# Performance work log

Measured on AMD Instinct MI355X. Metric: run time of the kernel, lower is better.

## Reference

```python
import jax
import jax.numpy as jnp
import numpy as np

N = 1024   # n_neurons (input size == hidden size)
L = 2      # n_layers of the stacked nn.RNN
T = 8      # n_tsteps (number of chained RNN+Linear blocks)
B = 1024   # x.shape[0]; acts as the RNN sequence length (batch=1 inside nn.RNN)


def setup_inputs() -> dict:
    key = jax.random.key(0)
    ks = jax.random.split(key, 7)
    s = 1.0 / np.sqrt(N)  # torch default init bound for RNN/Linear with fan_in=N
    x = jax.random.normal(ks[0], (B, T, N), dtype=jnp.float32)
    rnn_Wih = jax.random.uniform(ks[1], (T, L, N, N), minval=-s, maxval=s, dtype=jnp.float32)
    rnn_Whh = jax.random.uniform(ks[2], (T, L, N, N), minval=-s, maxval=s, dtype=jnp.float32)
    rnn_bih = jax.random.uniform(ks[3], (T, L, N), minval=-s, maxval=s, dtype=jnp.float32)
    rnn_bhh = jax.random.uniform(ks[4], (T, L, N), minval=-s, maxval=s, dtype=jnp.float32)
    lin_W = jax.random.uniform(ks[5], (T, N, N), minval=-s, maxval=s, dtype=jnp.float32)
    lin_b = jax.random.uniform(ks[6], (T, N), minval=-s, maxval=s, dtype=jnp.float32)
    return {"x": x, "rnn_Wih": rnn_Wih, "rnn_Whh": rnn_Whh,
            "rnn_bih": rnn_bih, "rnn_bhh": rnn_bhh,
            "lin_W": lin_W, "lin_b": lin_b}


def _rnn_layer(seq, Wih, Whh, bih, bhh):
    """Single tanh-RNN layer over sequence `seq` [S, N] with batch=1, h0=0."""
    def step(h, xt):
        h_new = jnp.tanh(xt @ Wih.T + bih + h @ Whh.T + bhh)
        return h_new, h_new
    _, out = jax.lax.scan(step, jnp.zeros((Wih.shape[0],), seq.dtype), seq)
    return out  # [S, N]


def reference(x, rnn_Wih, rnn_Whh, rnn_bih, rnn_bhh, lin_W, lin_b):
    # x: [B, T, N]. Torch code feeds x[:, 0, :] (shape [B, 1, N]) into nn.RNN
    # (batch_first=False), so B is the sequence length and batch size is 1.
    n_tsteps, n_layers = rnn_Wih.shape[0], rnn_Wih.shape[1]
    seq = x[:, 0, :]  # [B, N]
    outs = []
    for t in range(n_tsteps):
        for l in range(n_layers):
            seq = _rnn_layer(seq, rnn_Wih[t, l], rnn_Whh[t, l],
                             rnn_bih[t, l], rnn_bhh[t, l])
        seq = seq @ lin_W[t].T + lin_b[t]  # nn.Linear
        outs.append(seq)
    return jnp.stack(outs, axis=1)  # [B, T, N]
```

## Files before the change

### kernel.cpp

```cpp
#include <hip/hip_runtime.h>
#include <hip/hip_fp16.h>

#define NN 1024
#define NST 16

typedef _Float16 v2h __attribute__((ext_vector_type(2)));
typedef _Float16 f16x8 __attribute__((ext_vector_type(8)));
typedef float f32x4 __attribute__((ext_vector_type(4)));
typedef unsigned int uint;
typedef unsigned long long u64;
typedef unsigned int u32x4 __attribute__((ext_vector_type(4)));

__device__ __half g_W[NST][NN][2048];
__device__ float g_bias[NST][NN];
__device__ u64 g_S[NST][NN][512];
__device__ float g_Hout[8][NN * NN];
__device__ _Float16 g_Wih16F[7][NN * NN];
__device__ _Float16 g_linW16[8][NN * NN];

__device__ __forceinline__ v2h as_v2h(uint u) {
  union { uint u; v2h h; } c; c.u = u; return c.h;
}
__device__ __forceinline__ uint pk2(float a, float b) {
  union { v2h h; uint u; } c; c.h.x = (_Float16)a; c.h.y = (_Float16)b; return c.u;
}
__device__ __forceinline__ int swzu(int u) {
  return (u & ~7) | ((u + (u >> 3)) & 7);
}
__device__ __forceinline__ u32x4 ld_opaque16(const __half* p) {
  u32x4 r;
  asm volatile("global_load_dwordx4 %0, %1, off" : "=v"(r) : "v"(p));
  return r;
}
__device__ __forceinline__ float fdot4(u32x4 w, u32x4 v, float a) {
  a = __builtin_amdgcn_fdot2(as_v2h(w.x), as_v2h(v.x), a, false);
  a = __builtin_amdgcn_fdot2(as_v2h(w.y), as_v2h(v.y), a, false);
  a = __builtin_amdgcn_fdot2(as_v2h(w.z), as_v2h(v.z), a, false);
  a = __builtin_amdgcn_fdot2(as_v2h(w.w), as_v2h(v.w), a, false);
  return a;
}
__device__ __forceinline__ float dpp_reduce16(float v) {
  int t;
  t = __builtin_amdgcn_update_dpp(0, __float_as_int(v), 0x111, 0xF, 0xF, true); v += __int_as_float(t);
  t = __builtin_amdgcn_update_dpp(0, __float_as_int(v), 0x112, 0xF, 0xF, true); v += __int_as_float(t);
  t = __builtin_amdgcn_update_dpp(0, __float_as_int(v), 0x114, 0xF, 0xF, true); v += __int_as_float(t);
  t = __builtin_amdgcn_update_dpp(0, __float_as_int(v), 0x118, 0xF, 0xF, true); v += __int_as_float(t);
  return v;
}

__global__ void k_init() {
  const size_t n = (size_t)NST * NN * 512;
  size_t i = (size_t)blockIdx.x * blockDim.x + threadIdx.x;
  const size_t stride = (size_t)gridDim.x * blockDim.x;
  u64* p = &g_S[0][0][0];
  for (; i < n; i += stride) p[i] = 0ull;
}

__global__ void k_pack(const float* __restrict__ Wih, const float* __restrict__ Whh,
                       const float* __restrict__ linW) {
  const size_t total = (size_t)NST * NN * NN;
  const size_t stride = (size_t)gridDim.x * blockDim.x;
  for (size_t i = (size_t)blockIdx.x * blockDim.x + threadIdx.x; i < total; i += stride) {
    const int st = (int)(i >> 20);
    const int m = (int)(i >> 10) & 1023;
    const int k = (int)i & 1023;
    g_W[st][m][1024 + k] = __float2half(Whh[i]);
    const int t = st >> 1, l = st & 1;
    if (l == 1 || t == 0) g_W[st][m][k] = __float2half(Wih[i]);
    else g_Wih16F[t - 1][(size_t)m * NN + k] = (_Float16)Wih[i];
  }
  const size_t ltotal = (size_t)8 * NN * NN;
  _Float16* lw = &g_linW16[0][0];
  for (size_t i = (size_t)blockIdx.x * blockDim.x + threadIdx.x; i < ltotal; i += stride)
    lw[i] = (_Float16)linW[i];
}

#define GPAD 40

__global__ __launch_bounds__(256) void k_fold(int dummy) {
  const int tm1 = blockIdx.z;
  const int st = (tm1 + 1) * 2;
  const _Float16* A = &g_Wih16F[tm1][0];
  const _Float16* B = &g_linW16[tm1][0];
  __shared__ _Float16 sA[128 * GPAD];
  __shared__ _Float16 sB[128 * GPAD];
  const int tid = threadIdx.x;
  const int bm = blockIdx.y << 7, bn = blockIdx.x << 7;
  const int lane = tid & 63, wid = tid >> 6;
  const int wm = wid >> 1, wn = wid & 1;
  const int lr = lane & 15, kc = (lane >> 4) << 3;
  f32x4 acc[4][4] = {};
  const int arow = tid >> 1, ahalf = tid & 1;
  const int bj = tid >> 3, bcs = tid & 7;

  for (int k0 = 0; k0 < NN; k0 += 32) {
    __syncthreads();
    {
      const u32x4 a0 = *(const u32x4*)&A[(size_t)(bm + arow) * NN + k0 + 16 * ahalf];
      const u32x4 a1 = *(const u32x4*)&A[(size_t)(bm + arow) * NN + k0 + 16 * ahalf + 8];
      u32x4* dst = (u32x4*)&sA[arow * GPAD + 16 * ahalf];
      dst[0] = a0; dst[1] = a1;
      union { u32x4 v; _Float16 h[8]; } ua, ub;
      ua.v = *(const u32x4*)&B[(size_t)(k0 + bj) * NN + bn + 16 * bcs];
      ub.v = *(const u32x4*)&B[(size_t)(k0 + bj) * NN + bn + 16 * bcs + 8];
      #pragma unroll
      for (int q = 0; q < 8; ++q) sB[(16 * bcs + q) * GPAD + bj] = ua.h[q];
      #pragma unroll
      for (int q = 0; q < 8; ++q) sB[(16 * bcs + 8 + q) * GPAD + bj] = ub.h[q];
    }
    __syncthreads();
    f16x8 af[4], bf[4];
    #pragma unroll
    for (int f = 0; f < 4; ++f) {
      af[f] = *(const f16x8*)&sA[(wm * 64 + f * 16 + lr) * GPAD + kc];
      bf[f] = *(const f16x8*)&sB[(wn * 64 + f * 16 + lr) * GPAD + kc];
    }
    #pragma unroll
    for (int fm = 0; fm < 4; ++fm)
      #pragma unroll
      for (int fn = 0; fn < 4; ++fn)
        acc[fm][fn] = __builtin_amdgcn_mfma_f32_16x16x32_f16(af[fm], bf[fn], acc[fm][fn], 0, 0, 0);
  }
  const int orow = (lane >> 4) << 2, ocol = lane & 15;
  #pragma unroll
  for (int fm = 0; fm < 4; ++fm)
    #pragma unroll
    for (int fn = 0; fn < 4; ++fn) {
      const int gr = bm + wm * 64 + fm * 16 + orow;
      const int gc = bn + wn * 64 + fn * 16 + ocol;
      #pragma unroll
      for (int r = 0; r < 4; ++r)
        g_W[st][gr + r][gc] = __float2half(acc[fm][fn][r]);
    }
}

__global__ __launch_bounds__(256) void k_out(const float* __restrict__ linb,
                                             float* __restrict__ out) {
  const int t = blockIdx.z;
  const float* A = &g_Hout[t][0];
  const _Float16* B = &g_linW16[t][0];
  __shared__ _Float16 sA[128 * GPAD];
  __shared__ _Float16 sB[128 * GPAD];
  const int tid = threadIdx.x;
  const int bm = blockIdx.y << 7, bn = blockIdx.x << 7;
  const int lane = tid & 63, wid = tid >> 6;
  const int wm = wid >> 1, wn = wid & 1;
  const int lr = lane & 15, kc = (lane >> 4) << 3;
  f32x4 acc[4][4] = {};
  const int arow = tid >> 1, ahalf = tid & 1;

  for (int k0 = 0; k0 < NN; k0 += 32) {
    __syncthreads();
    {
      const float* srcA = &A[(size_t)(bm + arow) * NN + k0 + 16 * ahalf];
      const float4 f0 = *(const float4*)&srcA[0];
      const float4 f1 = *(const float4*)&srcA[4];
      const float4 f2 = *(const float4*)&srcA[8];
      const float4 f3 = *(const float4*)&srcA[12];
      u32x4 o0, o1;
      o0.x = pk2(f0.x, f0.y); o0.y = pk2(f0.z, f0.w);
      o0.z = pk2(f1.x, f1.y); o0.w = pk2(f1.z, f1.w);
      o1.x = pk2(f2.x, f2.y); o1.y = pk2(f2.z, f2.w);
      o1.z = pk2(f3.x, f3.y); o1.w = pk2(f3.z, f3.w);
      u32x4* dstA = (u32x4*)&sA[arow * GPAD + 16 * ahalf];
      dstA[0] = o0; dstA[1] = o1;
      const u32x4 b0 = *(const u32x4*)&B[(size_t)(bn + arow) * NN + k0 + 16 * ahalf];
      const u32x4 b1 = *(const u32x4*)&B[(size_t)(bn + arow) * NN + k0 + 16 * ahalf + 8];
      u32x4* dstB = (u32x4*)&sB[arow * GPAD + 16 * ahalf];
      dstB[0] = b0; dstB[1] = b1;
    }
    __syncthreads();
    f16x8 af[4], bf[4];
    #pragma unroll
    for (int f = 0; f < 4; ++f) {
      af[f] = *(const f16x8*)&sA[(wm * 64 + f * 16 + lr) * GPAD + kc];
      bf[f] = *(const f16x8*)&sB[(wn * 64 + f * 16 + lr) * GPAD + kc];
    }
    #pragma unroll
    for (int fm = 0; fm < 4; ++fm)
      #pragma unroll
      for (int fn = 0; fn < 4; ++fn)
        acc[fm][fn] = __builtin_amdgcn_mfma_f32_16x16x32_f16(af[fm], bf[fn], acc[fm][fn], 0, 0, 0);
  }
  const int orow = (lane >> 4) << 2, ocol = lane & 15;
  #pragma unroll
  for (int fm = 0; fm < 4; ++fm)
    #pragma unroll
    for (int fn = 0; fn < 4; ++fn) {
      const int gr = bm + wm * 64 + fm * 16 + orow;
      const int gc = bn + wn * 64 + fn * 16 + ocol;
      const float lb = linb[(size_t)t * NN + gc];
      #pragma unroll
      for (int r = 0; r < 4; ++r)
        out[(size_t)(gr + r) * 8192 + (size_t)t * NN + gc] = acc[fm][fn][r] + lb;
    }
}

__global__ __launch_bounds__(256) void k_bias(const float* __restrict__ Wih,
    const float* __restrict__ bih, const float* __restrict__ bhh,
    const float* __restrict__ linb) {
  const int st = blockIdx.x, t = st >> 1, l = st & 1;
  const int tid = threadIdx.x;
  const int m = (blockIdx.y << 8) + tid;
  __shared__ float slb[NN];
  const bool folded = (l == 0 && t > 0);
  if (folded)
    for (int k = tid; k < NN; k += 256) slb[k] = linb[(size_t)(t - 1) * NN + k];
  __syncthreads();
  float b = bih[(size_t)st * NN + m] + bhh[(size_t)st * NN + m];
  if (folded) {
    const float* wr = Wih + (size_t)st * NN * NN + (size_t)m * NN;
    float s0 = 0, s1 = 0, s2 = 0, s3 = 0;
    for (int k = 0; k < NN; k += 4) {
      const float4 w = *(const float4*)&wr[k];
      s0 += w.x * slb[k]; s1 += w.y * slb[k + 1];
      s2 += w.z * slb[k + 2]; s3 += w.w * slb[k + 3];
    }
    b += (s0 + s1) + (s2 + s3);
  }
  g_bias[st][m] = b;
}

__global__ __launch_bounds__(512)
__attribute__((amdgpu_waves_per_eu(2, 2)))
void k_phase(const float* __restrict__ x) {
  __shared__ __align__(16) unsigned char comb[2][4096];
  const int tid = threadIdx.x;
  const int bid = blockIdx.x;
  const int st = ((bid & 7) << 1) + (bid >> 7);
  const int wg = (bid >> 3) & 15;
  const int woff = wg << 6;
  const int i = tid >> 4;
  const int c = tid & 15;

#define LDX(RR, JJ) ld_opaque16(&g_W[st][woff + 2 * i + (RR)][64 * c + 8 * (JJ)])
#define LDH(RR, JJ) ld_opaque16(&g_W[st][woff + 2 * i + (RR)][1024 + 64 * c + 8 * (JJ)])
  u32x4 x00 = LDX(0,0), x01 = LDX(0,1), x02 = LDX(0,2), x03 = LDX(0,3);
  u32x4 x04 = LDX(0,4), x05 = LDX(0,5), x06 = LDX(0,6), x07 = LDX(0,7);
  u32x4 x10 = LDX(1,0), x11 = LDX(1,1), x12 = LDX(1,2), x13 = LDX(1,3);
  u32x4 x14 = LDX(1,4), x15 = LDX(1,5), x16 = LDX(1,6), x17 = LDX(1,7);
  u32x4 h00 = LDH(0,0), h01 = LDH(0,1), h02 = LDH(0,2), h03 = LDH(0,3);
  u32x4 h04 = LDH(0,4), h05 = LDH(0,5), h06 = LDH(0,6), h07 = LDH(0,7);
  u32x4 h10 = LDH(1,0), h11 = LDH(1,1), h12 = LDH(1,2), h13 = LDH(1,3);
  u32x4 h14 = LDH(1,4), h15 = LDH(1,5), h16 = LDH(1,6), h17 = LDH(1,7);
#undef LDX
#undef LDH
  asm volatile("s_waitcnt vmcnt(0)" ::: "memory");
  __builtin_amdgcn_sched_barrier(0);

  const float2 breg = *(const float2*)&g_bias[st][woff + 2 * i];

  const int uW = tid >> 2, off4 = (tid & 3) << 2;
  const int wbx = swzu(uW) * 16 + off4;
  const int wbh = swzu(128 + uW) * 16 + off4;
  const int slot_pub = (woff >> 1) + i;

  for (int s = 0; s < NN; ++s) {
    unsigned char* cb = comb[s & 1];
    uint xu = 0;
    if (st == 0) {
      const float2 xv = *(const float2*)&x[(size_t)s * 8192 + 2 * tid];
      xu = pk2(xv.x, xv.y);
    } else {
      const u64* pu = &g_S[st - 1][s][tid];
      for (;;) {
        const u64 a = __hip_atomic_load(pu, __ATOMIC_RELAXED, __HIP_MEMORY_SCOPE_AGENT);
        if (a >> 32) { xu = (uint)a; break; }
        __builtin_amdgcn_s_sleep(1);
      }
    }
    *(uint*)&cb[wbx] = xu;
    __syncthreads();

    float p0 = 0.f, p1 = 0.f;
#define XSTEP(JJ, Q0, Q1) { \
      const u32x4 v = *(const u32x4*)&cb[swzu(8 * c + (JJ)) * 16]; \
      p0 = fdot4(Q0, v, p0); p1 = fdot4(Q1, v, p1); }
    XSTEP(0, x00, x10) XSTEP(1, x01, x11) XSTEP(2, x02, x12) XSTEP(3, x03, x13)
    XSTEP(4, x04, x14) XSTEP(5, x05, x15) XSTEP(6, x06, x16) XSTEP(7, x07, x17)
#undef XSTEP

    uint hu = 0;
    if (s > 0) {
      const u64* po = &g_S[st][s - 1][tid];
      for (;;) {
        const u64 b = __hip_atomic_load(po, __ATOMIC_RELAXED, __HIP_MEMORY_SCOPE_AGENT);
        if (b >> 32) { hu = (uint)b; break; }
      }
    }
    *(uint*)&cb[wbh] = hu;
    __syncthreads();

#define HSTEP(JJ, Q0, Q1) { \
      const u32x4 v = *(const u32x4*)&cb[swzu(128 + 8 * c + (JJ)) * 16]; \
      p0 = fdot4(Q0, v, p0); p1 = fdot4(Q1, v, p1); }
    HSTEP(0, h00, h10) HSTEP(1, h01, h11) HSTEP(2, h02, h12) HSTEP(3, h03, h13)
    HSTEP(4, h04, h14) HSTEP(5, h05, h15) HSTEP(6, h06, h16) HSTEP(7, h07, h17)
#undef HSTEP

    p0 = dpp_reduce16(p0);
    p1 = dpp_reduce16(p1);
    if (c == 15) {
      const float hv0 = tanhf(p0 + breg.x);
      const float hv1 = tanhf(p1 + breg.y);
      const u64 pv = (1ull << 32) | (u64)pk2(hv0, hv1);
      __hip_atomic_store(&g_S[st][s][slot_pub], pv,
                         __ATOMIC_RELAXED, __HIP_MEMORY_SCOPE_AGENT);
      if (st & 1)
        *(float2*)&g_Hout[st >> 1][(size_t)s * NN + woff + 2 * i] =
            make_float2(hv0, hv1);
    }
  }
}

extern "C" void kernel_launch(void* const* d_in, const int* in_sizes, int n_in,
                              void* d_out, int out_size, void* d_ws, size_t ws_size,
                              hipStream_t stream) {
  (void)in_sizes; (void)n_in; (void)out_size; (void)d_ws; (void)ws_size;
  const float* x    = (const float*)d_in[0];
  const float* Wih  = (const float*)d_in[1];
  const float* Whh  = (const float*)d_in[2];
  const float* bih  = (const float*)d_in[3];
  const float* bhh  = (const float*)d_in[4];
  const float* linW = (const float*)d_in[5];
  const float* linb = (const float*)d_in[6];
  float* out = (float*)d_out;

  k_init<<<2048, 256, 0, stream>>>();
  k_pack<<<2048, 256, 0, stream>>>(Wih, Whh, linW);
  k_fold<<<dim3(8, 8, 7), 256, 0, stream>>>(0);
  k_bias<<<dim3(16, 4), 256, 0, stream>>>(Wih, bih, bhh, linb);
  k_phase<<<256, 512, 0, stream>>>(x);
  k_out<<<dim3(8, 8, 8), 256, 0, stream>>>(linb, out);
}
```

Measured before the change: 1.969 ms.

## Remap recurrent matvec to 4 rows per 32-lane group with shared LDS vector reuse

```diff
diff --git a/kernel.cpp b/kernel.cpp
--- a/kernel.cpp
+++ b/kernel.cpp
@@ -39,12 +39,13 @@
   a = __builtin_amdgcn_fdot2(as_v2h(w.w), as_v2h(v.w), a, false);
   return a;
 }
-__device__ __forceinline__ float dpp_reduce16(float v) {
+__device__ __forceinline__ float dpp_reduce32(float v) {
   int t;
   t = __builtin_amdgcn_update_dpp(0, __float_as_int(v), 0x111, 0xF, 0xF, true); v += __int_as_float(t);
   t = __builtin_amdgcn_update_dpp(0, __float_as_int(v), 0x112, 0xF, 0xF, true); v += __int_as_float(t);
   t = __builtin_amdgcn_update_dpp(0, __float_as_int(v), 0x114, 0xF, 0xF, true); v += __int_as_float(t);
   t = __builtin_amdgcn_update_dpp(0, __float_as_int(v), 0x118, 0xF, 0xF, true); v += __int_as_float(t);
+  t = __builtin_amdgcn_update_dpp(0, __float_as_int(v), 0x142, 0xF, 0xF, true); v += __int_as_float(t);
   return v;
 }
 
@@ -230,30 +231,36 @@
   const int st = ((bid & 7) << 1) + (bid >> 7);
   const int wg = (bid >> 3) & 15;
   const int woff = wg << 6;
-  const int i = tid >> 4;
-  const int c = tid & 15;
-
-#define LDX(RR, JJ) ld_opaque16(&g_W[st][woff + 2 * i + (RR)][64 * c + 8 * (JJ)])
-#define LDH(RR, JJ) ld_opaque16(&g_W[st][woff + 2 * i + (RR)][1024 + 64 * c + 8 * (JJ)])
-  u32x4 x00 = LDX(0,0), x01 = LDX(0,1), x02 = LDX(0,2), x03 = LDX(0,3);
-  u32x4 x04 = LDX(0,4), x05 = LDX(0,5), x06 = LDX(0,6), x07 = LDX(0,7);
-  u32x4 x10 = LDX(1,0), x11 = LDX(1,1), x12 = LDX(1,2), x13 = LDX(1,3);
-  u32x4 x14 = LDX(1,4), x15 = LDX(1,5), x16 = LDX(1,6), x17 = LDX(1,7);
-  u32x4 h00 = LDH(0,0), h01 = LDH(0,1), h02 = LDH(0,2), h03 = LDH(0,3);
-  u32x4 h04 = LDH(0,4), h05 = LDH(0,5), h06 = LDH(0,6), h07 = LDH(0,7);
-  u32x4 h10 = LDH(1,0), h11 = LDH(1,1), h12 = LDH(1,2), h13 = LDH(1,3);
-  u32x4 h14 = LDH(1,4), h15 = LDH(1,5), h16 = LDH(1,6), h17 = LDH(1,7);
+  const int i = tid >> 5;
+  const int c = tid & 31;
+  const int row0 = woff + 4 * i;
+
+#define LDX(RR, JJ) ld_opaque16(&g_W[st][row0 + (RR)][32 * c + 8 * (JJ)])
+#define LDH(RR, JJ) ld_opaque16(&g_W[st][row0 + (RR)][1024 + 32 * c + 8 * (JJ)])
+  u32x4 a00 = LDX(0,0), a01 = LDX(0,1), a02 = LDX(0,2), a03 = LDX(0,3);
+  u32x4 a10 = LDX(1,0), a11 = LDX(1,1), a12 = LDX(1,2), a13 = LDX(1,3);
+  u32x4 a20 = LDX(2,0), a21 = LDX(2,1), a22 = LDX(2,2), a23 = LDX(2,3);
+  u32x4 a30 = LDX(3,0), a31 = LDX(3,1), a32 = LDX(3,2), a33 = LDX(3,3);
+  u32x4 b00 = LDH(0,0), b01 = LDH(0,1), b02 = LDH(0,2), b03 = LDH(0,3);
+  u32x4 b10 = LDH(1,0), b11 = LDH(1,1), b12 = LDH(1,2), b13 = LDH(1,3);
+  u32x4 b20 = LDH(2,0), b21 = LDH(2,1), b22 = LDH(2,2), b23 = LDH(2,3);
+  u32x4 b30 = LDH(3,0), b31 = LDH(3,1), b32 = LDH(3,2), b33 = LDH(3,3);
 #undef LDX
 #undef LDH
   asm volatile("s_waitcnt vmcnt(0)" ::: "memory");
   __builtin_amdgcn_sched_barrier(0);
 
-  const float2 breg = *(const float2*)&g_bias[st][woff + 2 * i];
+  const float4 ba = *(const float4*)&g_bias[st][row0];
 
   const int uW = tid >> 2, off4 = (tid & 3) << 2;
   const int wbx = swzu(uW) * 16 + off4;
   const int wbh = swzu(128 + uW) * 16 + off4;
-  const int slot_pub = (woff >> 1) + i;
+  const int rx0 = swzu(4 * c + 0) * 16, rx1 = swzu(4 * c + 1) * 16;
+  const int rx2 = swzu(4 * c + 2) * 16, rx3 = swzu(4 * c + 3) * 16;
+  const int rh0 = swzu(128 + 4 * c + 0) * 16, rh1 = swzu(128 + 4 * c + 1) * 16;
+  const int rh2 = swzu(128 + 4 * c + 2) * 16, rh3 = swzu(128 + 4 * c + 3) * 16;
+  const int slot0 = (woff >> 1) + 2 * i;
+  const bool isPub = (c == 31);
 
   for (int s = 0; s < NN; ++s) {
     unsigned char* cb = comb[s & 1];
@@ -272,13 +279,17 @@
     *(uint*)&cb[wbx] = xu;
     __syncthreads();
 
-    float p0 = 0.f, p1 = 0.f;
-#define XSTEP(JJ, Q0, Q1) { \
-      const u32x4 v = *(const u32x4*)&cb[swzu(8 * c + (JJ)) * 16]; \
-      p0 = fdot4(Q0, v, p0); p1 = fdot4(Q1, v, p1); }
-    XSTEP(0, x00, x10) XSTEP(1, x01, x11) XSTEP(2, x02, x12) XSTEP(3, x03, x13)
-    XSTEP(4, x04, x14) XSTEP(5, x05, x15) XSTEP(6, x06, x16) XSTEP(7, x07, x17)
-#undef XSTEP
+    float p0, p1, p2, p3;
+    {
+      const u32x4 v0 = *(const u32x4*)&cb[rx0];
+      const u32x4 v1 = *(const u32x4*)&cb[rx1];
+      const u32x4 v2 = *(const u32x4*)&cb[rx2];
+      const u32x4 v3 = *(const u32x4*)&cb[rx3];
+      p0 = fdot4(a03, v3, fdot4(a02, v2, fdot4(a01, v1, fdot4(a00, v0, 0.f))));
+      p1 = fdot4(a13, v3, fdot4(a12, v2, fdot4(a11, v1, fdot4(a10, v0, 0.f))));
+      p2 = fdot4(a23, v3, fdot4(a22, v2, fdot4(a21, v1, fdot4(a20, v0, 0.f))));
+      p3 = fdot4(a33, v3, fdot4(a32, v2, fdot4(a31, v1, fdot4(a30, v0, 0.f))));
+    }
 
     uint hu = 0;
     if (s > 0) {
@@ -291,24 +302,34 @@
     *(uint*)&cb[wbh] = hu;
     __syncthreads();
 
-#define HSTEP(JJ, Q0, Q1) { \
-      const u32x4 v = *(const u32x4*)&cb[swzu(128 + 8 * c + (JJ)) * 16]; \
-      p0 = fdot4(Q0, v, p0); p1 = fdot4(Q1, v, p1); }
-    HSTEP(0, h00, h10) HSTEP(1, h01, h11) HSTEP(2, h02, h12) HSTEP(3, h03, h13)
-    HSTEP(4, h04, h14) HSTEP(5, h05, h15) HSTEP(6, h06, h16) HSTEP(7, h07, h17)
-#undef HSTEP
-
-    p0 = dpp_reduce16(p0);
-    p1 = dpp_reduce16(p1);
-    if (c == 15) {
-      const float hv0 = tanhf(p0 + breg.x);
-      const float hv1 = tanhf(p1 + breg.y);
-      const u64 pv = (1ull << 32) | (u64)pk2(hv0, hv1);
-      __hip_atomic_store(&g_S[st][s][slot_pub], pv,
+    {
+      const u32x4 v0 = *(const u32x4*)&cb[rh0];
+      const u32x4 v1 = *(const u32x4*)&cb[rh1];
+      const u32x4 v2 = *(const u32x4*)&cb[rh2];
+      const u32x4 v3 = *(const u32x4*)&cb[rh3];
+      p0 = fdot4(b03, v3, fdot4(b02, v2, fdot4(b01, v1, fdot4(b00, v0, p0))));
+      p1 = fdot4(b13, v3, fdot4(b12, v2, fdot4(b11, v1, fdot4(b10, v0, p1))));
+      p2 = fdot4(b23, v3, fdot4(b22, v2, fdot4(b21, v1, fdot4(b20, v0, p2))));
+      p3 = fdot4(b33, v3, fdot4(b32, v2, fdot4(b31, v1, fdot4(b30, v0, p3))));
+    }
+
+    p0 = dpp_reduce32(p0);
+    p1 = dpp_reduce32(p1);
+    p2 = dpp_reduce32(p2);
+    p3 = dpp_reduce32(p3);
+    if (isPub) {
+      const float h0 = tanhf(p0 + ba.x);
+      const float h1 = tanhf(p1 + ba.y);
+      const float h2 = tanhf(p2 + ba.z);
+      const float h3 = tanhf(p3 + ba.w);
+      u64* sp = &g_S[st][s][slot0];
+      __hip_atomic_store(&sp[0], (1ull << 32) | (u64)pk2(h0, h1),
+                         __ATOMIC_RELAXED, __HIP_MEMORY_SCOPE_AGENT);
+      __hip_atomic_store(&sp[1], (1ull << 32) | (u64)pk2(h2, h3),
                          __ATOMIC_RELAXED, __HIP_MEMORY_SCOPE_AGENT);
       if (st & 1)
-        *(float2*)&g_Hout[st >> 1][(size_t)s * NN + woff + 2 * i] =
-            make_float2(hv0, hv1);
+        *(float4*)&g_Hout[st >> 1][(size_t)s * NN + row0] =
+            make_float4(h0, h1, h2, h3);
     }
   }
 }
```

Result: slower. 2.664 ms (+35.3%).
